# Kernel optimization log

Hardware: AMD Instinct MI355X
Metric: run time of the kernel (lower is better)

Reference implementation:

```python
import jax, jax.numpy as jnp
import numpy as np

TIME_SCALES = [1, 2, 4]
K = len(TIME_SCALES)      # 3 scales
N = 4                     # lcm(time_scales)
S = sum(TIME_SCALES)      # 7 slots
D_HEAD = 128              # d
D = S * D_HEAD            # 896
IO_DIM = 1024
RANK = 64
HIDDEN = 4 * D            # 3584
EPS = 1e-5


def _tables():
    active = np.empty((N, K), dtype=np.int64)
    perm = np.empty((N, K, N), dtype=np.int64)
    inv = np.empty((N, K, N), dtype=np.int64)
    ids = np.arange(N)
    for ph in range(N):
        off = 0
        for k, s in enumerate(TIME_SCALES):
            active[ph, k] = off + ph % s
            off += s
            j = ph % s
            alpha = N // s
            p = (ids + alpha * j) % N   # SHARED assignment
            perm[ph, k] = p
            ip = np.empty_like(p)
            ip[p] = ids
            inv[ph, k] = ip
    return active, perm, inv

ACTIVE, PERM, INV = _tables()


def _ln(x, scale, bias):
    mu = jnp.mean(x, axis=-1, keepdims=True)
    var = jnp.mean((x - mu) ** 2, axis=-1, keepdims=True)
    return (x - mu) * jax.lax.rsqrt(var + EPS) * scale + bias


def setup_inputs() -> dict:
    key = jax.random.key(0)
    ks = jax.random.split(key, 16)
    B, T = 8, 1024

    def w(k, shape, s=0.02):
        return jax.random.normal(k, shape, dtype=jnp.float32) * s

    return {
        "x": jax.random.normal(ks[0], (B, T, IO_DIM), dtype=jnp.float32),
        "enc_base_w": w(ks[1], (D, IO_DIM)),
        "enc_A_w": w(ks[2], (RANK, IO_DIM)),
        "enc_B": w(ks[3], (RANK, N, D)),
        "enc_beta": jnp.float32(0.01),
        "Wqkv": w(ks[4], (K, N, D_HEAD, 3 * D_HEAD)),
        "ln_attn_scale": jnp.ones((D_HEAD,), jnp.float32),
        "ln_attn_bias": jnp.zeros((D_HEAD,), jnp.float32),
        "ln_mixer_scale": jnp.ones((D,), jnp.float32),
        "ln_mixer_bias": jnp.zeros((D,), jnp.float32),
        "mixer_w1": w(ks[5], (HIDDEN, D)),
        "mixer_b1": jnp.zeros((HIDDEN,), jnp.float32),
        "mixer_w2": w(ks[6], (D, HIDDEN)),
        "mixer_b2": jnp.zeros((D,), jnp.float32),
        "dec_ln_scale": jnp.ones((N * D,), jnp.float32),
        "dec_ln_bias": jnp.zeros((N * D,), jnp.float32),
        "dec_down_w": w(ks[7], (RANK, N * D)),
        "dec_up_w": w(ks[8], (IO_DIM, RANK)),
        "phase": 1,
    }


def reference(x, enc_base_w, enc_A_w, enc_B, enc_beta, Wqkv,
              ln_attn_scale, ln_attn_bias, ln_mixer_scale, ln_mixer_bias,
              mixer_w1, mixer_b1, mixer_w2, mixer_b2,
              dec_ln_scale, dec_ln_bias, dec_down_w, dec_up_w, phase):
    B, T, _ = x.shape
    # ---- StreamLoRAEncoder: x [B,T,io] -> z0 [B,T,N,D]
    base = x @ enc_base_w.T                 # [B,T,D]
    h = x @ enc_A_w.T                       # [B,T,r]
    delta = jnp.einsum('btr,rnd->btnd', h, enc_B)
    z0 = base[:, :, None, :] + enc_beta * delta
    # ---- gather active slots for this phase (one slot per scale group)
    slots = ACTIVE[phase]                   # [K]
    z_slots = z0.reshape(B, T, N, S, D_HEAD)
    x_slot = z_slots[:, :, :, slots, :]     # [B,T,N,K,d]
    x_slot = _ln(x_slot, ln_attn_scale, ln_attn_bias)
    # ---- SHARED qkv projection (stream->head inverse perm, bmm, head->stream perm)
    x_in = x_slot.transpose(0, 1, 3, 2, 4)  # [B,T,K,N,d]
    kk = np.arange(K)[:, None]
    x_head = x_in[:, :, kk, INV[phase], :]  # [B,T,K,N,d]
    qkv = jnp.einsum('btknd,knde->btkne', x_head, Wqkv)  # [B,T,K,N,3d]
    qh, kh, vh = jnp.split(qkv, 3, axis=-1)
    p = PERM[phase]
    q = qh[:, :, kk, p, :].transpose(0, 3, 2, 1, 4).reshape(B, N * K, T, D_HEAD)
    k_ = kh[:, :, kk, p, :].transpose(0, 3, 2, 1, 4).reshape(B, N * K, T, D_HEAD)
    v = vh[:, :, kk, p, :].transpose(0, 3, 2, 1, 4).reshape(B, N * K, T, D_HEAD)
    # ---- causal attention over T per (stream, scale) head
    scores = jnp.einsum('bhtd,bhsd->bhts', q, k_) / np.float32(np.sqrt(D_HEAD))
    mask = jnp.tril(jnp.ones((T, T), dtype=bool))
    scores = jnp.where(mask, scores, jnp.float32(-1e9))
    attn = jax.nn.softmax(scores, axis=-1)
    out = jnp.einsum('bhts,bhsd->bhtd', attn, v)  # [B,N*K,T,d]
    # ---- scatter back to active slots (residual add)
    out5 = out.reshape(B, N, K, T, D_HEAD).transpose(0, 3, 1, 2, 4)  # [B,T,N,K,d]
    z1 = z_slots.at[:, :, :, slots, :].add(out5).reshape(B, T, N, D)
    # ---- mixer MLP (pre-LN residual)
    hm = _ln(z1, ln_mixer_scale, ln_mixer_bias)
    m = jax.nn.gelu(hm @ mixer_w1.T + mixer_b1, approximate=False) @ mixer_w2.T + mixer_b2
    z2 = z1 + m
    # ---- StreamLoRADecoder: concat streams, LN, rank-bottleneck projection
    cat = z2.reshape(B, T, N * D)
    y = _ln(cat, dec_ln_scale, dec_ln_bias) @ dec_down_w.T @ dec_up_w.T
    return y
```

## Files before the change

### kernel.cpp

```cpp
#include <hip/hip_runtime.h>
#include <hip/hip_bf16.h>
#include <math.h>


#define BT   8192
#define DH   128
#define DD   896
#define ND   3584
#define IO   1024
#define RK   64
#define HID  3584

typedef __attribute__((ext_vector_type(8))) short short8;
typedef __attribute__((ext_vector_type(4))) float f32x4;
typedef __hip_bfloat16 bf16;

#define DS_READ_B128(dst, p)                                                  \
    asm volatile("ds_read_b128 %0, %1"                                        \
                 : "=v"(dst)                                                  \
                 : "v"((const __attribute__((address_space(3))) bf16*)(p)))

__device__ __forceinline__ float gelu_f(float v)
{
    float u = v * 0.70710678118654752f;
    float a = fabsf(u);
    float t = __builtin_amdgcn_rcpf(1.0f + 0.3275911f * a);
    float p = t * (0.254829592f + t * (-0.284496736f + t * (1.421413741f +
              t * (-1.453152027f + t * 1.061405429f))));
    float er = 1.0f - p * __expf(-u * u);
    er = copysignf(er, u);
    return 0.5f * v * (1.0f + er);
}

template<int BM, int BN, int BK, int TM, int TN>
__global__ __launch_bounds__(256) void gemm_kernel(const float* __restrict__ A,
                                                   const float* __restrict__ B,
                                                   float* __restrict__ C,
                                                   int N, int Kd)
{
    constexpr int THREADS = (BM / TM) * (BN / TN);
    constexpr int LDA = BM + 4;
    constexpr int LDB = BN + 4;
    __shared__ float As[BK][LDA];
    __shared__ float Bs[BK][LDB];

    const int tid = threadIdx.x;
    constexpr int NX = BN / TN;
    const int tx = tid % NX;
    const int ty = tid / NX;
    const int row0 = blockIdx.y * BM;
    const int col0 = blockIdx.x * BN;

    float acc[TM][TN];
#pragma unroll
    for (int i = 0; i < TM; ++i)
#pragma unroll
        for (int j = 0; j < TN; ++j) acc[i][j] = 0.f;

    for (int k0 = 0; k0 < Kd; k0 += BK) {
        constexpr int AF4 = BM * BK / 4;
        for (int f = tid; f < AF4; f += THREADS) {
            int r  = f / (BK / 4);
            int c4 = (f % (BK / 4)) * 4;
            float4 v = *(const float4*)(A + (size_t)(row0 + r) * Kd + k0 + c4);
            As[c4 + 0][r] = v.x; As[c4 + 1][r] = v.y;
            As[c4 + 2][r] = v.z; As[c4 + 3][r] = v.w;
        }
        constexpr int BF4 = BN * BK / 4;
        for (int f = tid; f < BF4; f += THREADS) {
            int r  = f / (BK / 4);
            int c4 = (f % (BK / 4)) * 4;
            float4 v = *(const float4*)(B + (size_t)(col0 + r) * Kd + k0 + c4);
            Bs[c4 + 0][r] = v.x; Bs[c4 + 1][r] = v.y;
            Bs[c4 + 2][r] = v.z; Bs[c4 + 3][r] = v.w;
        }
        __syncthreads();

#pragma unroll
        for (int kk = 0; kk < BK; ++kk) {
            float a[TM], b[TN];
#pragma unroll
            for (int i = 0; i < TM; i += 4)
                *(float4*)&a[i] = *(const float4*)&As[kk][ty * TM + i];
#pragma unroll
            for (int j = 0; j < TN; j += 4)
                *(float4*)&b[j] = *(const float4*)&Bs[kk][tx * TN + j];
#pragma unroll
            for (int i = 0; i < TM; ++i)
#pragma unroll
                for (int j = 0; j < TN; ++j)
                    acc[i][j] = fmaf(a[i], b[j], acc[i][j]);
        }
        __syncthreads();
    }

    const int crow = row0 + ty * TM;
    const int ccol = col0 + tx * TN;
#pragma unroll
    for (int i = 0; i < TM; ++i) {
        float* cp = C + (size_t)(crow + i) * N + ccol;
#pragma unroll
        for (int j = 0; j < TN; ++j) cp[j] = acc[i][j];
    }
}

template<int SPLIT>
__global__ __launch_bounds__(256) void gemm_splitk_kernel(const float* __restrict__ A,
                                                          const float* __restrict__ B,
                                                          float* __restrict__ C,
                                                          int N, int ld)
{
    __shared__ float As[16][68];
    __shared__ float Bs[16][68];
    const int tid = threadIdx.x;
    const int tx = tid & 15, ty = tid >> 4;
    const int row0 = blockIdx.y * 64;
    const int col0 = blockIdx.x * 64;
    const int kn   = ld / SPLIT;
    const int kbeg = blockIdx.z * kn;

    float acc[4][4];
#pragma unroll
    for (int i = 0; i < 4; ++i)
#pragma unroll
        for (int j = 0; j < 4; ++j) acc[i][j] = 0.f;

    for (int k0 = kbeg; k0 < kbeg + kn; k0 += 16) {
        {
            int r = tid >> 2, c4 = (tid & 3) << 2;
            float4 v = *(const float4*)(A + (size_t)(row0 + r) * ld + k0 + c4);
            As[c4 + 0][r] = v.x; As[c4 + 1][r] = v.y;
            As[c4 + 2][r] = v.z; As[c4 + 3][r] = v.w;
            float4 w = *(const float4*)(B + (size_t)(col0 + r) * ld + k0 + c4);
            Bs[c4 + 0][r] = w.x; Bs[c4 + 1][r] = w.y;
            Bs[c4 + 2][r] = w.z; Bs[c4 + 3][r] = w.w;
        }
        __syncthreads();
#pragma unroll
        for (int kk = 0; kk < 16; ++kk) {
            float a[4], b[4];
            *(float4*)a = *(const float4*)&As[kk][ty * 4];
            *(float4*)b = *(const float4*)&Bs[kk][tx * 4];
#pragma unroll
            for (int i = 0; i < 4; ++i)
#pragma unroll
                for (int j = 0; j < 4; ++j)
                    acc[i][j] = fmaf(a[i], b[j], acc[i][j]);
        }
        __syncthreads();
    }

#pragma unroll
    for (int i = 0; i < 4; ++i)
#pragma unroll
        for (int j = 0; j < 4; ++j)
            atomicAdd(C + (size_t)(row0 + ty * 4 + i) * N + col0 + tx * 4 + j,
                      acc[i][j]);
}

template<int BN, int EPI>
__global__ __launch_bounds__(512, 2) void gemm_bf16_256(
    const bf16* __restrict__ A,
    const bf16* __restrict__ B,
    float* __restrict__ Cf,
    bf16* __restrict__ Cb,
    int N, int Kd,
    const float* __restrict__ bias)
{
    constexpr int NR    = BN / 64;
    constexpr int WTN   = 16 * NR;
    constexpr int ASLOT = 256 * 32;
    constexpr int BSLOT = BN * 32;
    __shared__ bf16 As[4 * ASLOT];
    __shared__ bf16 Bs[4 * BSLOT];

    const int tid  = threadIdx.x;
    const int wave = tid >> 6;
    const int lane = tid & 63;
    const int wm = wave >> 2, wn = wave & 3;
    const int lr = lane & 15, lq = lane >> 4;

    const int gx  = gridDim.x;
    int fid = blockIdx.y * gx + blockIdx.x;
    const int cpx = (gx * gridDim.y) >> 3;
    fid = (fid & 7) * cpx + (fid >> 3);
    const int row0 = (fid / gx) * 256;
    const int col0 = (fid % gx) * BN;

    const int sr  = lane >> 2;
    const int scs = (((lane & 3) ^ ((lane >> 3) & 3)) << 3);
    const bf16* Ag = A + (size_t)(row0 + sr) * Kd + scs;
    const bf16* Bg = B + (size_t)(col0 + sr) * Kd + scs;

    const int scox = (lq * 8) ^ (((lr >> 1) & 3) << 3);

    f32x4 acc[8][NR];
#pragma unroll
    for (int i = 0; i < 8; ++i)
#pragma unroll
        for (int j = 0; j < NR; ++j) acc[i][j] = (f32x4){0.f, 0.f, 0.f, 0.f};

    const int NH = Kd >> 5;

    auto stage = [&](int h) {
        const int slot = h & 3;
#pragma unroll
        for (int i = 0; i < 2; ++i) {
            const int rg = (i * 8 + wave) * 16;
            __builtin_amdgcn_global_load_lds(
                (const __attribute__((address_space(1))) unsigned int*)
                    (Ag + (size_t)rg * Kd + h * 32),
                (__attribute__((address_space(3))) unsigned int*)
                    (As + slot * ASLOT + rg * 32),
                16, 0, 0);
        }
#pragma unroll
        for (int i = 0; i < BN / 128; ++i) {
            const int rg = (i * 8 + wave) * 16;
            __builtin_amdgcn_global_load_lds(
                (const __attribute__((address_space(1))) unsigned int*)
                    (Bg + (size_t)rg * Kd + h * 32),
                (__attribute__((address_space(3))) unsigned int*)
                    (Bs + slot * BSLOT + rg * 32),
                16, 0, 0);
        }
    };

    stage(0); stage(1); stage(2);

    for (int h = 0; h < NH; ++h) {
        if (h + 3 < NH) stage(h + 3);

        const int ahead = NH - 1 - h;
        if constexpr (BN == 256) {
            if (ahead >= 3)      asm volatile("s_waitcnt vmcnt(12)" ::: "memory");
            else if (ahead == 2) asm volatile("s_waitcnt vmcnt(8)"  ::: "memory");
            else if (ahead == 1) asm volatile("s_waitcnt vmcnt(4)"  ::: "memory");
            else                 asm volatile("s_waitcnt vmcnt(0)"  ::: "memory");
        } else {
            if (ahead >= 3)      asm volatile("s_waitcnt vmcnt(9)"  ::: "memory");
            else if (ahead == 2) asm volatile("s_waitcnt vmcnt(6)"  ::: "memory");
            else if (ahead == 1) asm volatile("s_waitcnt vmcnt(3)"  ::: "memory");
            else                 asm volatile("s_waitcnt vmcnt(0)"  ::: "memory");
        }
        __builtin_amdgcn_s_barrier();

        const bf16* Ab = As + (h & 3) * ASLOT;
        const bf16* Bb = Bs + (h & 3) * BSLOT;

        short8 bfr[NR], afr[8];
#pragma unroll
        for (int nt = 0; nt < NR; ++nt)
            DS_READ_B128(bfr[nt], Bb + (wn * WTN + nt * 16 + lr) * 32 + scox);
#pragma unroll
        for (int mt = 0; mt < 8; ++mt)
            DS_READ_B128(afr[mt], Ab + (wm * 128 + mt * 16 + lr) * 32 + scox);

        asm volatile("s_waitcnt lgkmcnt(0)" ::: "memory");
        __builtin_amdgcn_sched_barrier(0);

        __builtin_amdgcn_s_setprio(1);
#pragma unroll
        for (int mt = 0; mt < 8; ++mt)
#pragma unroll
            for (int nt = 0; nt < NR; ++nt)
                acc[mt][nt] = __builtin_amdgcn_mfma_f32_16x16x32_bf16(
                    afr[mt], bfr[nt], acc[mt][nt], 0, 0, 0);
        __builtin_amdgcn_s_setprio(0);

        __builtin_amdgcn_s_barrier();
    }

#pragma unroll
    for (int mt = 0; mt < 8; ++mt) {
#pragma unroll
        for (int nt = 0; nt < NR; ++nt) {
            const int col = col0 + wn * WTN + nt * 16 + lr;
            const float bcol = (EPI == 0) ? 0.f : bias[col];
#pragma unroll
            for (int r = 0; r < 4; ++r) {
                const int row = row0 + wm * 128 + mt * 16 + lq * 4 + r;
                float v = acc[mt][nt][r] + bcol;
                if (EPI == 1) {
                    Cb[(size_t)row * N + col] = __float2bfloat16(gelu_f(v));
                } else if (EPI == 2) {
                    Cf[(size_t)row * N + col] += v;
                } else {
                    Cf[(size_t)row * N + col] = v;
                }
            }
        }
    }
}

__global__ __launch_bounds__(256) void pack_enc_kernel(const float* __restrict__ baseW,
                                                       const float* __restrict__ Aw,
                                                       const float* __restrict__ Bv,
                                                       const float* __restrict__ betap,
                                                       bf16* __restrict__ outp)
{
    __shared__ float Ps[64][68];
    __shared__ float Qs[64][68];
    const int tid = threadIdx.x;
    const int e0 = blockIdx.y * 64;
    const int k0 = blockIdx.x * 64;

    for (int f = tid; f < 1024; f += 256) {
        int r = f >> 4, c4 = (f & 15) << 2;
        *(float4*)&Ps[r][c4] = *(const float4*)(Bv + (size_t)r * ND + e0 + c4);
        *(float4*)&Qs[r][c4] = *(const float4*)(Aw + (size_t)r * IO + k0 + c4);
    }
    __syncthreads();

    const int tx = tid & 15, ty = tid >> 4;
    float acc[4][4];
#pragma unroll
    for (int i = 0; i < 4; ++i)
#pragma unroll
        for (int j = 0; j < 4; ++j) acc[i][j] = 0.f;

#pragma unroll 8
    for (int r = 0; r < 64; ++r) {
        float a[4], b[4];
        *(float4*)a = *(const float4*)&Ps[r][ty * 4];
        *(float4*)b = *(const float4*)&Qs[r][tx * 4];
#pragma unroll
        for (int i = 0; i < 4; ++i)
#pragma unroll
            for (int j = 0; j < 4; ++j) acc[i][j] = fmaf(a[i], b[j], acc[i][j]);
    }

    const float beta = betap[0];
#pragma unroll
    for (int i = 0; i < 4; ++i) {
        const int e = e0 + ty * 4 + i;
        const int d = e % DD;
#pragma unroll
        for (int j = 0; j < 4; ++j) {
            const int k = k0 + tx * 4 + j;
            float v = baseW[(size_t)d * IO + k] + beta * acc[i][j];
            outp[(size_t)e * IO + k] = __float2bfloat16(v);
        }
    }
}

__global__ __launch_bounds__(256) void qkv_bf16_kernel(
    const bf16* __restrict__ xh,
    const bf16* __restrict__ Wt,
    bf16* __restrict__ Qg,
    bf16* __restrict__ Kg,
    bf16* __restrict__ Vtg,
    const int* __restrict__ phase_p,
    int go)
{
    __shared__ bf16 As[128 * 64];
    __shared__ bf16 Bs[128 * 64];

    const int ph  = phase_p[0] & 3;
    const int zbl = blockIdx.z;
    const int hh  = (go + zbl) % 12;
    const int n   = hh / 3;
    const int k   = hh % 3;
    const int m   = (k == 0) ? n
                  : (k == 1) ? ((n + 2 * (ph & 1)) & 3)
                             : ((n + (ph & 3)) & 3);
    const bf16* A  = xh + (size_t)zbl * (1024 * 128);
    const bf16* Bw = Wt + (size_t)(k * 4 + m) * (384 * 128);

    const int tid  = threadIdx.x;
    const int wave = tid >> 6;
    const int lane = tid & 63;
    const int wm = wave >> 1, wn = wave & 1;
    const int row0 = blockIdx.y * 128;
    const int col0 = blockIdx.x * 128;
    const int lr = lane & 15;
    const int lq = lane >> 4;
    const int srow = lane >> 3;
    const int scol = (lane & 7) * 8;

    f32x4 acc[4][4];
#pragma unroll
    for (int i = 0; i < 4; ++i)
#pragma unroll
        for (int j = 0; j < 4; ++j) acc[i][j] = (f32x4){0.f, 0.f, 0.f, 0.f};

#pragma unroll
    for (int k0 = 0; k0 < 128; k0 += 64) {
#pragma unroll
        for (int j = 0; j < 4; ++j) {
            const int rg = wave * 32 + j * 8;
            __builtin_amdgcn_global_load_lds(
                (const __attribute__((address_space(1))) unsigned int*)
                    (A + (size_t)(row0 + rg + srow) * 128 + k0 + scol),
                (__attribute__((address_space(3))) unsigned int*)(As + rg * 64),
                16, 0, 0);
        }
#pragma unroll
        for (int j = 0; j < 4; ++j) {
            const int rg = wave * 32 + j * 8;
            __builtin_amdgcn_global_load_lds(
                (const __attribute__((address_space(1))) unsigned int*)
                    (Bw + (size_t)(col0 + rg + srow) * 128 + k0 + scol),
                (__attribute__((address_space(3))) unsigned int*)(Bs + rg * 64),
                16, 0, 0);
        }
        __syncthreads();

#pragma unroll
        for (int s = 0; s < 64; s += 32) {
            short8 af[4], bf[4];
#pragma unroll
            for (int mt = 0; mt < 4; ++mt)
                af[mt] = *(const short8*)&As[(wm * 64 + mt * 16 + lr) * 64 + s + lq * 8];
#pragma unroll
            for (int nt = 0; nt < 4; ++nt)
                bf[nt] = *(const short8*)&Bs[(wn * 64 + nt * 16 + lr) * 64 + s + lq * 8];
#pragma unroll
            for (int mt = 0; mt < 4; ++mt)
#pragma unroll
                for (int nt = 0; nt < 4; ++nt)
                    acc[mt][nt] = __builtin_amdgcn_mfma_f32_16x16x32_bf16(
                        af[mt], bf[nt], acc[mt][nt], 0, 0, 0);
        }
        __syncthreads();
    }

    if (col0 < 256) {
        bf16* C = (col0 == 0 ? Qg : Kg) + (size_t)zbl * (1024 * 128);
#pragma unroll
        for (int mt = 0; mt < 4; ++mt)
#pragma unroll
            for (int nt = 0; nt < 4; ++nt) {
                const int col = wn * 64 + nt * 16 + lr;
#pragma unroll
                for (int r = 0; r < 4; ++r) {
                    const int row = row0 + wm * 64 + mt * 16 + lq * 4 + r;
                    C[(size_t)row * 128 + col] = __float2bfloat16(acc[mt][nt][r]);
                }
            }
    } else {
        bf16* Vt = Vtg + (size_t)zbl * (128 * 1024);
#pragma unroll
        for (int mt = 0; mt < 4; ++mt)
#pragma unroll
            for (int nt = 0; nt < 4; ++nt) {
                const int d = wn * 64 + nt * 16 + lr;
                const int rowb = row0 + wm * 64 + mt * 16 + lq * 4;
                union { bf16 h[4]; uint2 u; } pk;
#pragma unroll
                for (int r = 0; r < 4; ++r)
                    pk.h[r] = __float2bfloat16(acc[mt][nt][r]);
                *(uint2*)(Vt + (size_t)d * 1024 + rowb) = pk.u;
            }
    }
}

__global__ __launch_bounds__(256, 2) void flash_bf16_kernel(
    const bf16* __restrict__ Qg,
    const bf16* __restrict__ Kg,
    const bf16* __restrict__ Vtg,
    float* __restrict__ z,
    const int* __restrict__ phase_p,
    int go, int GQ, int* __restrict__ cnt)
{
    __shared__ bf16 Ks[2 * 64 * 128];
    __shared__ bf16 Vs[2 * 128 * 64];
    __shared__ bf16 Ps[64 * 64];
    __shared__ int sw;

    const int ph   = phase_p[0] & 3;
    const int tid  = threadIdx.x;
    const int wave = tid >> 6;
    const int lane = tid & 63;
    const int lr = lane & 15;
    const int lq = lane >> 4;
    const int sr4 = lane >> 4, sc4 = (lane & 15) * 8;
    const int sr8 = lane >> 3, sc8 = (lane & 7) * 8;
    const int swz = (lr & 7) << 3;
    const float sc = 0.08838834764831845f;
    const int nitems = GQ * 16;

    for (;;) {
        if (tid == 0) sw = atomicAdd(cnt, 1);
        __syncthreads();
        const int w = sw;
        if (w >= nitems) return;

        const int wq  = w / GQ;
        const int qy  = 15 - wq;
        const int zbl = w - wq * GQ;
        const int zb  = go + zbl;
        const int b   = zb / 12;
        const int hh  = zb % 12;
        const int n   = hh / 3;
        const int ksl = hh % 3;
        const int slot = (ksl == 0) ? 0 : (ksl == 1 ? 1 + (ph & 1) : 3 + (ph & 3));
        const int q0  = qy * 64;

        const bf16* Qp = Qg  + (size_t)zbl * (1024 * 128);
        const bf16* Kp = Kg  + (size_t)zbl * (1024 * 128);
        const bf16* Vp = Vtg + (size_t)zbl * (128 * 1024);

        auto stageKV = [&](int t) {
            const int j0 = t * 64;
            bf16* Kd = Ks + (t & 1) * (64 * 128);
            bf16* Vd = Vs + (t & 1) * (128 * 64);
#pragma unroll
            for (int j = 0; j < 4; ++j) {
                const int rg = wave * 16 + j * 4;
                const int krow = rg + sr4;
                const int kcol = sc4 ^ ((krow & 7) << 3);
                __builtin_amdgcn_global_load_lds(
                    (const __attribute__((address_space(1))) unsigned int*)
                        (Kp + (size_t)(j0 + krow) * 128 + kcol),
                    (__attribute__((address_space(3))) unsigned int*)(Kd + rg * 128),
                    16, 0, 0);
            }
#pragma unroll
            for (int j = 0; j < 4; ++j) {
                const int rg = wave * 32 + j * 8;
                const int vrow = rg + sr8;
                const int vcol = sc8 ^ ((vrow & 7) << 3);
                __builtin_amdgcn_global_load_lds(
                    (const __attribute__((address_space(1))) unsigned int*)
                        (Vp + (size_t)vrow * 1024 + j0 + vcol),
                    (__attribute__((address_space(3))) unsigned int*)(Vd + rg * 64),
                    16, 0, 0);
            }
        };

        short8 qreg[4];
#pragma unroll
        for (int s = 0; s < 4; ++s)
            qreg[s] = *(const short8*)(Qp + (size_t)(q0 + wave * 16 + lr) * 128
                                       + s * 32 + lq * 8);

        f32x4 accO[8];
        float m_i[4], l_i[4];
#pragma unroll
        for (int j = 0; j < 8; ++j) accO[j] = (f32x4){0.f, 0.f, 0.f, 0.f};
#pragma unroll
        for (int r = 0; r < 4; ++r) { m_i[r] = -1e30f; l_i[r] = 0.f; }

        const int NT = qy + 1;
        stageKV(0);

        for (int t = 0; t < NT; ++t) {
            if (t + 1 < NT) {
                stageKV(t + 1);
                asm volatile("s_waitcnt vmcnt(8)" ::: "memory");
            } else {
                asm volatile("s_waitcnt vmcnt(0)" ::: "memory");
            }
            __builtin_amdgcn_s_barrier();
            __builtin_amdgcn_sched_barrier(0);

            const bf16* Kbb = Ks + (t & 1) * (64 * 128);
            const bf16* Vbb = Vs + (t & 1) * (128 * 64);
            const int j0 = t * 64;

            f32x4 accS[4];
#pragma unroll
            for (int nt = 0; nt < 4; ++nt) accS[nt] = (f32x4){0.f, 0.f, 0.f, 0.f};
            short8 bk[2][4];
#pragma unroll
            for (int nt = 0; nt < 4; ++nt)
                DS_READ_B128(bk[0][nt],
                             Kbb + (nt * 16 + lr) * 128 + ((lq * 8) ^ swz));
#pragma unroll
            for (int s = 0; s < 4; ++s) {
                if (s + 1 < 4) {
#pragma unroll
                    for (int nt = 0; nt < 4; ++nt)
                        DS_READ_B128(bk[(s + 1) & 1][nt],
                                     Kbb + (nt * 16 + lr) * 128
                                         + (((s + 1) * 32 + lq * 8) ^ swz));
                    asm volatile("s_waitcnt lgkmcnt(4)" ::: "memory");
                } else {
                    asm volatile("s_waitcnt lgkmcnt(0)" ::: "memory");
                }
                __builtin_amdgcn_sched_barrier(0);
#pragma unroll
                for (int nt = 0; nt < 4; ++nt)
                    accS[nt] = __builtin_amdgcn_mfma_f32_16x16x32_bf16(
                        qreg[s], bk[s & 1][nt], accS[nt], 0, 0, 0);
            }

            const bool need_mask = (t == NT - 1);
#pragma unroll
            for (int r = 0; r < 4; ++r) {
                const int row = q0 + wave * 16 + lq * 4 + r;
                float sv[4];
#pragma unroll
                for (int nt = 0; nt < 4; ++nt) {
                    float v = accS[nt][r] * sc;
                    if (need_mask && (j0 + nt * 16 + lr > row)) v = -1e30f;
                    sv[nt] = v;
                }
                float mx = fmaxf(fmaxf(sv[0], sv[1]), fmaxf(sv[2], sv[3]));
#pragma unroll
                for (int msk = 8; msk; msk >>= 1) mx = fmaxf(mx, __shfl_xor(mx, msk, 16));
                float mnew = fmaxf(m_i[r], mx);
                float al   = __expf(m_i[r] - mnew);
                float rs = 0.f;
#pragma unroll
                for (int nt = 0; nt < 4; ++nt) {
                    sv[nt] = __expf(sv[nt] - mnew);
                    rs += sv[nt];
                }
#pragma unroll
                for (int msk = 8; msk; msk >>= 1) rs += __shfl_xor(rs, msk, 16);
                l_i[r] = l_i[r] * al + rs;
                m_i[r] = mnew;
#pragma unroll
                for (int d8 = 0; d8 < 8; ++d8) accO[d8][r] *= al;
                const int prow = wave * 16 + lq * 4 + r;
                const int pswz = (prow & 7) << 3;
#pragma unroll
                for (int nt = 0; nt < 4; ++nt)
                    Ps[prow * 64 + ((nt * 16 + lr) ^ pswz)] = __float2bfloat16(sv[nt]);
            }
            asm volatile("" ::: "memory");
            __builtin_amdgcn_sched_barrier(0);

            short8 ap[2], bv[2][8];
            DS_READ_B128(ap[0], Ps + (wave * 16 + lr) * 64 + ((lq * 8) ^ swz));
#pragma unroll
            for (int d8 = 0; d8 < 8; ++d8)
                DS_READ_B128(bv[0][d8],
                             Vbb + (d8 * 16 + lr) * 64 + ((lq * 8) ^ swz));
#pragma unroll
            for (int kv = 0; kv < 2; ++kv) {
                if (kv == 0) {
                    DS_READ_B128(ap[1],
                                 Ps + (wave * 16 + lr) * 64 + ((32 + lq * 8) ^ swz));
#pragma unroll
                    for (int d8 = 0; d8 < 8; ++d8)
                        DS_READ_B128(bv[1][d8],
                                     Vbb + (d8 * 16 + lr) * 64 + ((32 + lq * 8) ^ swz));
                    asm volatile("s_waitcnt lgkmcnt(9)" ::: "memory");
                } else {
                    asm volatile("s_waitcnt lgkmcnt(0)" ::: "memory");
                }
                __builtin_amdgcn_sched_barrier(0);
#pragma unroll
                for (int d8 = 0; d8 < 8; ++d8)
                    accO[d8] = __builtin_amdgcn_mfma_f32_16x16x32_bf16(
                        ap[kv], bv[kv][d8], accO[d8], 0, 0, 0);
            }

            __builtin_amdgcn_s_barrier();
        }

#pragma unroll
        for (int r = 0; r < 4; ++r) {
            const int t = q0 + wave * 16 + lq * 4 + r;
            const float inv = 1.0f / l_i[r];
            float* dst = z + (size_t)(b * 1024 + t) * ND + n * DD + slot * DH;
#pragma unroll
            for (int d8 = 0; d8 < 8; ++d8)
                dst[d8 * 16 + lr] += accO[d8][r] * inv;
        }
    }
}

__global__ __launch_bounds__(256) void cvt_bf16_kernel(const float* __restrict__ src,
                                                       bf16* __restrict__ dst,
                                                       int n4)
{
    int i = blockIdx.x * 256 + threadIdx.x;
    if (i < n4) {
        float4 v = ((const float4*)src)[i];
        bf16* d = dst + (size_t)i * 4;
        d[0] = __float2bfloat16(v.x);
        d[1] = __float2bfloat16(v.y);
        d[2] = __float2bfloat16(v.z);
        d[3] = __float2bfloat16(v.w);
    }
}

__global__ __launch_bounds__(256) void cvt_wqkv_kernel(const float* __restrict__ W,
                                                       bf16* __restrict__ Wt)
{
    int o = blockIdx.x * 256 + threadIdx.x;
    if (o < 12 * 384 * 128) {
        int i = o / 49152, rem = o % 49152;
        int e = rem / 128, d = rem % 128;
        Wt[o] = __float2bfloat16(W[(size_t)i * 49152 + d * 384 + e]);
    }
}

__global__ __launch_bounds__(256) void ln_attn_kernel(const float* __restrict__ z,
                                                      bf16* __restrict__ xh,
                                                      const float* __restrict__ scale,
                                                      const float* __restrict__ bias,
                                                      const int* __restrict__ phase_p,
                                                      int bt0)
{
    const int ph   = phase_p[0] & 3;
    const int lane = threadIdx.x & 63;
    const int row  = blockIdx.x * 4 + (threadIdx.x >> 6);
    const int k    = row % 3;
    const int n    = (row / 3) & 3;
    const int btl  = row / 12;
    const int slot = (k == 0) ? 0 : (k == 1 ? 1 + (ph & 1) : 3 + (ph & 3));
    const int bt   = bt0 + btl;

    const float* src = z + (size_t)bt * ND + n * DD + slot * DH + lane * 2;
    float2 v = *(const float2*)src;
    float s = v.x + v.y;
    float q = v.x * v.x + v.y * v.y;
#pragma unroll
    for (int m = 32; m; m >>= 1) { s += __shfl_xor(s, m); q += __shfl_xor(q, m); }
    float mu  = s * (1.0f / 128.0f);
    float var = q * (1.0f / 128.0f) - mu * mu;
    float r   = rsqrtf(var + 1e-5f);

    float2 sc2 = *(const float2*)(scale + lane * 2);
    float2 bi2 = *(const float2*)(bias + lane * 2);
    const int bl = btl >> 10, t = btl & 1023;
    union { bf16 h[2]; unsigned int u; } pk;
    pk.h[0] = __float2bfloat16((v.x - mu) * r * sc2.x + bi2.x);
    pk.h[1] = __float2bfloat16((v.y - mu) * r * sc2.y + bi2.y);
    *(unsigned int*)(xh + (size_t)((bl * 12 + n * 3 + k) * 1024 + t) * DH + lane * 2) = pk.u;
}

template<int W>
__global__ __launch_bounds__(256) void ln_row_kernel(const float* __restrict__ in,
                                                     float* __restrict__ outp,
                                                     const float* __restrict__ scale,
                                                     const float* __restrict__ bias)
{
    constexpr int NIT = (W + 255) / 256;
    const int row = blockIdx.x;
    const int tid = threadIdx.x;
    const float* rp = in + (size_t)row * W;

    float v[NIT];
    float s = 0.f, q = 0.f;
#pragma unroll
    for (int i = 0; i < NIT; ++i) {
        int idx = tid + i * 256;
        if (idx < W) { float t = rp[idx]; v[i] = t; s += t; q += t * t; }
        else v[i] = 0.f;
    }
#pragma unroll
    for (int m = 32; m; m >>= 1) { s += __shfl_xor(s, m); q += __shfl_xor(q, m); }
    __shared__ float ss[4], sq[4];
    if ((tid & 63) == 0) { ss[tid >> 6] = s; sq[tid >> 6] = q; }
    __syncthreads();
    s = ss[0] + ss[1] + ss[2] + ss[3];
    q = sq[0] + sq[1] + sq[2] + sq[3];
    float mu  = s * (1.0f / W);
    float var = q * (1.0f / W) - mu * mu;
    float r   = rsqrtf(var + 1e-5f);

    float* op = outp + (size_t)row * W;
#pragma unroll
    for (int i = 0; i < NIT; ++i) {
        int idx = tid + i * 256;
        if (idx < W) op[idx] = (v[i] - mu) * r * scale[idx] + bias[idx];
    }
}

__global__ __launch_bounds__(256) void ln_row_bf16_kernel(const float* __restrict__ in,
                                                          bf16* __restrict__ outp,
                                                          const float* __restrict__ scale,
                                                          const float* __restrict__ bias)
{
    constexpr int W = 896, NIT = 4;
    const int row = blockIdx.x;
    const int tid = threadIdx.x;
    const float* rp = in + (size_t)row * W;

    float v[NIT];
    float s = 0.f, q = 0.f;
#pragma unroll
    for (int i = 0; i < NIT; ++i) {
        int idx = tid + i * 256;
        if (idx < W) { float t = rp[idx]; v[i] = t; s += t; q += t * t; }
        else v[i] = 0.f;
    }
#pragma unroll
    for (int m = 32; m; m >>= 1) { s += __shfl_xor(s, m); q += __shfl_xor(q, m); }
    __shared__ float ss[4], sq[4];
    if ((tid & 63) == 0) { ss[tid >> 6] = s; sq[tid >> 6] = q; }
    __syncthreads();
    s = ss[0] + ss[1] + ss[2] + ss[3];
    q = sq[0] + sq[1] + sq[2] + sq[3];
    float mu  = s * (1.0f / W);
    float var = q * (1.0f / W) - mu * mu;
    float r   = rsqrtf(var + 1e-5f);

    bf16* op = outp + (size_t)row * W;
#pragma unroll
    for (int i = 0; i < NIT; ++i) {
        int idx = tid + i * 256;
        if (idx < W)
            op[idx] = __float2bfloat16((v[i] - mu) * r * scale[idx] + bias[idx]);
    }
}

extern "C" void kernel_launch(void* const* d_in, const int* in_sizes, int n_in,
                              void* d_out, int out_size, void* d_ws, size_t ws_size,
                              hipStream_t stream)
{
    const float* x          = (const float*)d_in[0];
    const float* enc_base_w = (const float*)d_in[1];
    const float* enc_A_w    = (const float*)d_in[2];
    const float* enc_B      = (const float*)d_in[3];
    const float* enc_beta   = (const float*)d_in[4];
    const float* Wqkv       = (const float*)d_in[5];
    const float* ln_attn_s  = (const float*)d_in[6];
    const float* ln_attn_b  = (const float*)d_in[7];
    const float* ln_mix_s   = (const float*)d_in[8];
    const float* ln_mix_b   = (const float*)d_in[9];
    const float* w1         = (const float*)d_in[10];
    const float* b1         = (const float*)d_in[11];
    const float* w2         = (const float*)d_in[12];
    const float* b2         = (const float*)d_in[13];
    const float* dec_ln_s   = (const float*)d_in[14];
    const float* dec_ln_b   = (const float*)d_in[15];
    const float* dec_down   = (const float*)d_in[16];
    const float* dec_up     = (const float*)d_in[17];
    const int*   phase_p    = (const int*)d_in[18];
    float* out = (float*)d_out;

    float* ws = (float*)d_ws;
    float* z  = ws;
    float* R  = ws + (size_t)BT * ND;

    const int GQ = (ws_size >= 230000000UL) ? 96 : 48;
    const int CH = (ws_size >= 205000000UL) ? 8192 : 4096;

    bf16* xb   = (bf16*)R;
    bf16* Wenc = xb + (size_t)BT * IO;
    bf16* Wt   = (bf16*)R;
    bf16* xh_b = Wt + 12 * 384 * 128;
    bf16* Qb   = xh_b + (size_t)GQ * 1024 * 128;
    bf16* Kb   = Qb + (size_t)GQ * 1024 * 128;
    bf16* Vtg  = Kb + (size_t)GQ * 1024 * 128;
    int*  cnt  = (int*)(Vtg + (size_t)GQ * 128 * 1024);
    bf16* w1b  = (bf16*)R;
    bf16* w2b  = w1b + (size_t)HID * DD;
    bf16* hm   = w2b + (size_t)DD * HID;
    bf16* gbuf = hm + (size_t)CH * DD;
    float* t1  = R;

    cvt_bf16_kernel<<<dim3(8192), 256, 0, stream>>>(x, xb, BT * IO / 4);
    pack_enc_kernel<<<dim3(16, 56), 256, 0, stream>>>(enc_base_w, enc_A_w, enc_B,
                                                      enc_beta, Wenc);
    gemm_bf16_256<256, 0><<<dim3(14, 32), 512, 0, stream>>>(xb, Wenc, z, nullptr,
                                                            ND, IO, nullptr);

    cvt_wqkv_kernel<<<dim3(2304), 256, 0, stream>>>(Wqkv, Wt);
    hipMemsetAsync(cnt, 0, 2 * sizeof(int), stream);
    const int ngroups = 96 / GQ;
    for (int g = 0; g < ngroups; ++g) {
        ln_attn_kernel<<<dim3(GQ * 256), 256, 0, stream>>>(z, xh_b, ln_attn_s,
                                                           ln_attn_b, phase_p,
                                                           g * (GQ / 12) * 1024);
        qkv_bf16_kernel<<<dim3(3, 8, GQ), 256, 0, stream>>>(xh_b, Wt, Qb, Kb, Vtg,
                                                            phase_p, g * GQ);
        flash_bf16_kernel<<<dim3(512), 256, 0, stream>>>(Qb, Kb, Vtg, z,
                                                         phase_p, g * GQ, GQ,
                                                         cnt + g);
    }

    cvt_bf16_kernel<<<dim3(3136), 256, 0, stream>>>(w1, w1b, HID * DD / 4);
    cvt_bf16_kernel<<<dim3(3136), 256, 0, stream>>>(w2, w2b, DD * HID / 4);
    for (int c = 0; c < 32768 / CH; ++c) {
        float* zc = z + (size_t)c * CH * DD;
        ln_row_bf16_kernel<<<dim3(CH), 256, 0, stream>>>(zc, hm, ln_mix_s, ln_mix_b);
        gemm_bf16_256<256, 1><<<dim3(14, CH / 256), 512, 0, stream>>>(
            hm, w1b, nullptr, gbuf, HID, DD, b1);
        gemm_bf16_256<128, 2><<<dim3(7, CH / 256), 512, 0, stream>>>(
            gbuf, w2b, zc, nullptr, DD, HID, b2);
    }

    ln_row_kernel<3584><<<dim3(8192), 256, 0, stream>>>(z, z, dec_ln_s, dec_ln_b);
    hipMemsetAsync(t1, 0, (size_t)BT * RK * sizeof(float), stream);
    gemm_splitk_kernel<8><<<dim3(1, 128, 8), 256, 0, stream>>>(z, dec_down, t1,
                                                               RK, ND);
    gemm_kernel<128, 128, 16, 8, 8>
        <<<dim3(8, 64), 256, 0, stream>>>(t1, dec_up, out, IO, RK);
}
```

Before: 1.254 ms.

## Use 128-row query tiles with 8 waves in flash attention, single-buffered V

The flash attention kernel now runs 512 threads (8 waves) per block, and each work item covers 128 query rows instead of 64. Every K/V tile loaded into LDS is therefore shared by twice as many query rows, which halves K/V staging traffic per query. V is now single-buffered and staged one tile at a time alongside the next K prefetch, with an extra barrier between the score and PV phases. Waves whose rows lie entirely before the current key tile skip their work, but the block-wide barriers and the coarser work items add synchronisation and can leave load imbalance at the tail.

```diff
diff --git a/kernel.cpp b/kernel.cpp
--- a/kernel.cpp
+++ b/kernel.cpp
@@ -455,7 +455,7 @@
     }
 }
 
-__global__ __launch_bounds__(256, 2) void flash_bf16_kernel(
+__global__ __launch_bounds__(512, 4) void flash_bf16_kernel(
     const bf16* __restrict__ Qg,
     const bf16* __restrict__ Kg,
     const bf16* __restrict__ Vtg,
@@ -464,8 +464,8 @@
     int go, int GQ, int* __restrict__ cnt)
 {
     __shared__ bf16 Ks[2 * 64 * 128];
-    __shared__ bf16 Vs[2 * 128 * 64];
-    __shared__ bf16 Ps[64 * 64];
+    __shared__ bf16 Vs[128 * 64];
+    __shared__ bf16 Ps[128 * 64];
     __shared__ int sw;
 
     const int ph   = phase_p[0] & 3;
@@ -478,16 +478,17 @@
     const int sr8 = lane >> 3, sc8 = (lane & 7) * 8;
     const int swz = (lr & 7) << 3;
     const float sc = 0.08838834764831845f;
-    const int nitems = GQ * 16;
+    const int nitems = GQ * 8;
 
     for (;;) {
+        __syncthreads();
         if (tid == 0) sw = atomicAdd(cnt, 1);
         __syncthreads();
         const int w = sw;
         if (w >= nitems) return;
 
         const int wq  = w / GQ;
-        const int qy  = 15 - wq;
+        const int qy8 = 7 - wq;
         const int zbl = w - wq * GQ;
         const int zb  = go + zbl;
         const int b   = zb / 12;
@@ -495,19 +496,19 @@
         const int n   = hh / 3;
         const int ksl = hh % 3;
         const int slot = (ksl == 0) ? 0 : (ksl == 1 ? 1 + (ph & 1) : 3 + (ph & 3));
-        const int q0  = qy * 64;
+        const int q0  = qy8 * 128;
+        const int NT  = qy8 * 2 + 2;
 
         const bf16* Qp = Qg  + (size_t)zbl * (1024 * 128);
         const bf16* Kp = Kg  + (size_t)zbl * (1024 * 128);
         const bf16* Vp = Vtg + (size_t)zbl * (128 * 1024);
 
-        auto stageKV = [&](int t) {
+        auto stageK = [&](int t) {
             const int j0 = t * 64;
             bf16* Kd = Ks + (t & 1) * (64 * 128);
-            bf16* Vd = Vs + (t & 1) * (128 * 64);
-#pragma unroll
-            for (int j = 0; j < 4; ++j) {
-                const int rg = wave * 16 + j * 4;
+#pragma unroll
+            for (int j = 0; j < 2; ++j) {
+                const int rg = wave * 8 + j * 4;
                 const int krow = rg + sr4;
                 const int kcol = sc4 ^ ((krow & 7) << 3);
                 __builtin_amdgcn_global_load_lds(
@@ -516,15 +517,18 @@
                     (__attribute__((address_space(3))) unsigned int*)(Kd + rg * 128),
                     16, 0, 0);
             }
-#pragma unroll
-            for (int j = 0; j < 4; ++j) {
-                const int rg = wave * 32 + j * 8;
+        };
+        auto stageV = [&](int t) {
+            const int j0 = t * 64;
+#pragma unroll
+            for (int j = 0; j < 2; ++j) {
+                const int rg = wave * 16 + j * 8;
                 const int vrow = rg + sr8;
                 const int vcol = sc8 ^ ((vrow & 7) << 3);
                 __builtin_amdgcn_global_load_lds(
                     (const __attribute__((address_space(1))) unsigned int*)
                         (Vp + (size_t)vrow * 1024 + j0 + vcol),
-                    (__attribute__((address_space(3))) unsigned int*)(Vd + rg * 64),
+                    (__attribute__((address_space(3))) unsigned int*)(Vs + rg * 64),
                     16, 0, 0);
             }
         };
@@ -542,111 +546,117 @@
 #pragma unroll
         for (int r = 0; r < 4; ++r) { m_i[r] = -1e30f; l_i[r] = 0.f; }
 
-        const int NT = qy + 1;
-        stageKV(0);
+        stageK(0);
 
         for (int t = 0; t < NT; ++t) {
-            if (t + 1 < NT) {
-                stageKV(t + 1);
-                asm volatile("s_waitcnt vmcnt(8)" ::: "memory");
-            } else {
-                asm volatile("s_waitcnt vmcnt(0)" ::: "memory");
-            }
+            const bool more = (t + 1 < NT);
+            if (more) stageK(t + 1);
+            stageV(t);
+            if (more) asm volatile("s_waitcnt vmcnt(4)" ::: "memory");
+            else      asm volatile("s_waitcnt vmcnt(2)" ::: "memory");
             __builtin_amdgcn_s_barrier();
             __builtin_amdgcn_sched_barrier(0);
 
             const bf16* Kbb = Ks + (t & 1) * (64 * 128);
-            const bf16* Vbb = Vs + (t & 1) * (128 * 64);
             const int j0 = t * 64;
-
-            f32x4 accS[4];
-#pragma unroll
-            for (int nt = 0; nt < 4; ++nt) accS[nt] = (f32x4){0.f, 0.f, 0.f, 0.f};
-            short8 bk[2][4];
-#pragma unroll
-            for (int nt = 0; nt < 4; ++nt)
-                DS_READ_B128(bk[0][nt],
-                             Kbb + (nt * 16 + lr) * 128 + ((lq * 8) ^ swz));
-#pragma unroll
-            for (int s = 0; s < 4; ++s) {
-                if (s + 1 < 4) {
+            const bool active = (j0 <= q0 + wave * 16 + 15);
+
+            if (active) {
+                f32x4 accS[4];
+#pragma unroll
+                for (int nt = 0; nt < 4; ++nt) accS[nt] = (f32x4){0.f, 0.f, 0.f, 0.f};
+                short8 bk[2][4];
+#pragma unroll
+                for (int nt = 0; nt < 4; ++nt)
+                    DS_READ_B128(bk[0][nt],
+                                 Kbb + (nt * 16 + lr) * 128 + ((lq * 8) ^ swz));
+#pragma unroll
+                for (int s = 0; s < 4; ++s) {
+                    if (s + 1 < 4) {
+#pragma unroll
+                        for (int nt = 0; nt < 4; ++nt)
+                            DS_READ_B128(bk[(s + 1) & 1][nt],
+                                         Kbb + (nt * 16 + lr) * 128
+                                             + (((s + 1) * 32 + lq * 8) ^ swz));
+                        asm volatile("s_waitcnt lgkmcnt(4)" ::: "memory");
+                    } else {
+                        asm volatile("s_waitcnt lgkmcnt(0)" ::: "memory");
+                    }
+                    __builtin_amdgcn_sched_barrier(0);
 #pragma unroll
                     for (int nt = 0; nt < 4; ++nt)
-                        DS_READ_B128(bk[(s + 1) & 1][nt],
-                                     Kbb + (nt * 16 + lr) * 128
-                                         + (((s + 1) * 32 + lq * 8) ^ swz));
-                    asm volatile("s_waitcnt lgkmcnt(4)" ::: "memory");
-                } else {
-                    asm volatile("s_waitcnt lgkmcnt(0)" ::: "memory");
+                        accS[nt] = __builtin_amdgcn_mfma_f32_16x16x32_bf16(
+                            qreg[s], bk[s & 1][nt], accS[nt], 0, 0, 0);
                 }
-                __builtin_amdgcn_sched_barrier(0);
-#pragma unroll
-                for (int nt = 0; nt < 4; ++nt)
-                    accS[nt] = __builtin_amdgcn_mfma_f32_16x16x32_bf16(
-                        qreg[s], bk[s & 1][nt], accS[nt], 0, 0, 0);
+
+                const bool need_mask = (j0 + 63 > q0 + wave * 16);
+#pragma unroll
+                for (int r = 0; r < 4; ++r) {
+                    const int row = q0 + wave * 16 + lq * 4 + r;
+                    float sv[4];
+#pragma unroll
+                    for (int nt = 0; nt < 4; ++nt) {
+                        float v = accS[nt][r] * sc;
+                        if (need_mask && (j0 + nt * 16 + lr > row)) v = -1e30f;
+                        sv[nt] = v;
+                    }
+                    float mx = fmaxf(fmaxf(sv[0], sv[1]), fmaxf(sv[2], sv[3]));
+#pragma unroll
+                    for (int msk = 8; msk; msk >>= 1) mx = fmaxf(mx, __shfl_xor(mx, msk, 16));
+                    float mnew = fmaxf(m_i[r], mx);
+                    float al   = __expf(m_i[r] - mnew);
+                    float rs = 0.f;
+#pragma unroll
+                    for (int nt = 0; nt < 4; ++nt) {
+                        sv[nt] = __expf(sv[nt] - mnew);
+                        rs += sv[nt];
+                    }
+#pragma unroll
+                    for (int msk = 8; msk; msk >>= 1) rs += __shfl_xor(rs, msk, 16);
+                    l_i[r] = l_i[r] * al + rs;
+                    m_i[r] = mnew;
+#pragma unroll
+                    for (int d8 = 0; d8 < 8; ++d8) accO[d8][r] *= al;
+                    const int prow = wave * 16 + lq * 4 + r;
+                    const int pswz = (prow & 7) << 3;
+#pragma unroll
+                    for (int nt = 0; nt < 4; ++nt)
+                        Ps[prow * 64 + ((nt * 16 + lr) ^ pswz)] = __float2bfloat16(sv[nt]);
+                }
+                asm volatile("" ::: "memory");
             }
 
-            const bool need_mask = (t == NT - 1);
-#pragma unroll
-            for (int r = 0; r < 4; ++r) {
-                const int row = q0 + wave * 16 + lq * 4 + r;
-                float sv[4];
-#pragma unroll
-                for (int nt = 0; nt < 4; ++nt) {
-                    float v = accS[nt][r] * sc;
-                    if (need_mask && (j0 + nt * 16 + lr > row)) v = -1e30f;
-                    sv[nt] = v;
+            if (more) asm volatile("s_waitcnt vmcnt(2)" ::: "memory");
+            else      asm volatile("s_waitcnt vmcnt(0)" ::: "memory");
+            __builtin_amdgcn_s_barrier();
+            __builtin_amdgcn_sched_barrier(0);
+
+            if (active) {
+                short8 ap[2], bv[2][8];
+                DS_READ_B128(ap[0], Ps + (wave * 16 + lr) * 64 + ((lq * 8) ^ swz));
+#pragma unroll
+                for (int d8 = 0; d8 < 8; ++d8)
+                    DS_READ_B128(bv[0][d8],
+                                 Vs + (d8 * 16 + lr) * 64 + ((lq * 8) ^ swz));
+#pragma unroll
+                for (int kv = 0; kv < 2; ++kv) {
+                    if (kv == 0) {
+                        DS_READ_B128(ap[1],
+                                     Ps + (wave * 16 + lr) * 64 + ((32 + lq * 8) ^ swz));
+#pragma unroll
+                        for (int d8 = 0; d8 < 8; ++d8)
+                            DS_READ_B128(bv[1][d8],
+                                         Vs + (d8 * 16 + lr) * 64 + ((32 + lq * 8) ^ swz));
+                        asm volatile("s_waitcnt lgkmcnt(9)" ::: "memory");
+                    } else {
+                        asm volatile("s_waitcnt lgkmcnt(0)" ::: "memory");
+                    }
+                    __builtin_amdgcn_sched_barrier(0);
+#pragma unroll
+                    for (int d8 = 0; d8 < 8; ++d8)
+                        accO[d8] = __builtin_amdgcn_mfma_f32_16x16x32_bf16(
+                            ap[kv], bv[kv][d8], accO[d8], 0, 0, 0);
                 }
-                float mx = fmaxf(fmaxf(sv[0], sv[1]), fmaxf(sv[2], sv[3]));
-#pragma unroll
-                for (int msk = 8; msk; msk >>= 1) mx = fmaxf(mx, __shfl_xor(mx, msk, 16));
-                float mnew = fmaxf(m_i[r], mx);
-                float al   = __expf(m_i[r] - mnew);
-                float rs = 0.f;
-#pragma unroll
-                for (int nt = 0; nt < 4; ++nt) {
-                    sv[nt] = __expf(sv[nt] - mnew);
-                    rs += sv[nt];
-                }
-#pragma unroll
-                for (int msk = 8; msk; msk >>= 1) rs += __shfl_xor(rs, msk, 16);
-                l_i[r] = l_i[r] * al + rs;
-                m_i[r] = mnew;
-#pragma unroll
-                for (int d8 = 0; d8 < 8; ++d8) accO[d8][r] *= al;
-                const int prow = wave * 16 + lq * 4 + r;
-                const int pswz = (prow & 7) << 3;
-#pragma unroll
-                for (int nt = 0; nt < 4; ++nt)
-                    Ps[prow * 64 + ((nt * 16 + lr) ^ pswz)] = __float2bfloat16(sv[nt]);
-            }
-            asm volatile("" ::: "memory");
-            __builtin_amdgcn_sched_barrier(0);
-
-            short8 ap[2], bv[2][8];
-            DS_READ_B128(ap[0], Ps + (wave * 16 + lr) * 64 + ((lq * 8) ^ swz));
-#pragma unroll
-            for (int d8 = 0; d8 < 8; ++d8)
-                DS_READ_B128(bv[0][d8],
-                             Vbb + (d8 * 16 + lr) * 64 + ((lq * 8) ^ swz));
-#pragma unroll
-            for (int kv = 0; kv < 2; ++kv) {
-                if (kv == 0) {
-                    DS_READ_B128(ap[1],
-                                 Ps + (wave * 16 + lr) * 64 + ((32 + lq * 8) ^ swz));
-#pragma unroll
-                    for (int d8 = 0; d8 < 8; ++d8)
-                        DS_READ_B128(bv[1][d8],
-                                     Vbb + (d8 * 16 + lr) * 64 + ((32 + lq * 8) ^ swz));
-                    asm volatile("s_waitcnt lgkmcnt(9)" ::: "memory");
-                } else {
-                    asm volatile("s_waitcnt lgkmcnt(0)" ::: "memory");
-                }
-                __builtin_amdgcn_sched_barrier(0);
-#pragma unroll
-                for (int d8 = 0; d8 < 8; ++d8)
-                    accO[d8] = __builtin_amdgcn_mfma_f32_16x16x32_bf16(
-                        ap[kv], bv[kv][d8], accO[d8], 0, 0, 0);
             }
 
             __builtin_amdgcn_s_barrier();
@@ -862,7 +872,7 @@
                                                            g * (GQ / 12) * 1024);
         qkv_bf16_kernel<<<dim3(3, 8, GQ), 256, 0, stream>>>(xh_b, Wt, Qb, Kb, Vtg,
                                                             phase_p, g * GQ);
-        flash_bf16_kernel<<<dim3(512), 256, 0, stream>>>(Qb, Kb, Vtg, z,
+        flash_bf16_kernel<<<dim3(512), 512, 0, stream>>>(Qb, Kb, Vtg, z,
                                                          phase_p, g * GQ, GQ,
                                                          cnt + g);
     }
```

Measured after the change: 1.379 ms. 1.1x slower.
